# Kernel tuning notes

Hardware: AMD Instinct MI355X
Metric: run time of the kernel (lower is better)

## Reference

```python
import jax, jax.numpy as jnp
import numpy as np

N = 20000      # nodes
E = 160000     # edges
F_IN = 128     # num_node_features
D = 128        # embedding_size (out_channels)
H = 4          # heads
NEG = 0.2      # GATv2Conv negative_slope
N_LAYERS = 3


def setup_inputs() -> dict:
    key = jax.random.key(0)
    ks = jax.random.split(key, 12)
    s = 0.05
    return {
        "x": jax.random.normal(ks[0], (N, F_IN), jnp.float32),
        "edge_index": jax.random.randint(ks[1], (2, E), 0, N, jnp.int64),
        "edge_attr": jax.random.normal(ks[2], (E, 2), jnp.float32),
        "Wf": jax.random.normal(ks[3], (F_IN, D), jnp.float32) * s,
        "bf": jnp.zeros((D,), jnp.float32),
        "Wl": jax.random.normal(ks[4], (D, H * D), jnp.float32) * s,
        "bl": jnp.zeros((H * D,), jnp.float32),
        "Wr": jax.random.normal(ks[5], (D, H * D), jnp.float32) * s,
        "br": jnp.zeros((H * D,), jnp.float32),
        "We": jax.random.normal(ks[6], (2, H * D), jnp.float32) * s,
        "att": jax.random.normal(ks[7], (H, D), jnp.float32) * s,
        "bias_out": jnp.zeros((D,), jnp.float32),
    }


def reference(x, edge_index, edge_attr, Wf, bf, Wl, bl, Wr, br, We, att, bias_out):
    src, dst = edge_index[0], edge_index[1]

    # add_self_loops with fill_value='mean': self-loop edge_attr = mean of
    # incoming edge_attr per node (0 where a node has no incoming edges)
    ea_sum = jax.ops.segment_sum(edge_attr, dst, num_segments=N)            # [N,2]
    cnt = jax.ops.segment_sum(jnp.ones((E,), edge_attr.dtype), dst, num_segments=N)
    loop_attr = ea_sum / jnp.maximum(cnt, 1.0)[:, None]
    loop_idx = jnp.arange(N, dtype=src.dtype)
    fsrc = jnp.concatenate([src, loop_idx])                                  # [E+N]
    fdst = jnp.concatenate([dst, loop_idx])
    fea = jnp.concatenate([edge_attr, loop_attr], axis=0)                    # [E+N,2]

    ee = (fea @ We).reshape(-1, H, D)                                        # [E+N,H,D]

    def gatv2_layer(h):
        xl = (h @ Wl + bl).reshape(N, H, D)   # lin_l -> source-side / message
        xr = (h @ Wr + br).reshape(N, H, D)   # lin_r -> target-side
        e = jax.nn.leaky_relu(xl[fsrc] + xr[fdst] + ee, NEG)                 # [E+N,H,D]
        logits = jnp.einsum('ehd,hd->eh', e, att)                            # [E+N,H]
        m = jax.ops.segment_max(logits, fdst, num_segments=N)                # [N,H]
        w = jnp.exp(logits - m[fdst])
        denom = jax.ops.segment_sum(w, fdst, num_segments=N)                 # [N,H]
        alpha = w / denom[fdst]                                              # segment softmax
        msg = xl[fsrc] * alpha[..., None]                                    # [E+N,H,D]
        out = jax.ops.segment_sum(msg, fdst, num_segments=N)                 # [N,H,D]
        return out.mean(axis=1) + bias_out                                   # concat=False

    h = x @ Wf + bf
    for _ in range(N_LAYERS):
        h = jax.nn.leaky_relu(gatv2_layer(h), 0.01)  # F.leaky_relu default slope
    return h
```

## Files before the change

### kernel.cpp

```cpp
#include <hip/hip_runtime.h>
#include <hip/hip_bf16.h>

#define NN 20000
#define NE 160000
#define EF (NE + NN)
#define DD 128
#define HH 4
#define NPA (NN * DD)
#define NPW (1024 * 128 + 128 * 128 + 1024)
#define DEGB ((NE + 255) / 256)

typedef unsigned short u16;
typedef unsigned int u32;

using short8  = __attribute__((ext_vector_type(8))) short;
using float4v = __attribute__((ext_vector_type(4))) float;

__device__ __forceinline__ float bf2f(u16 u) {
    union { u32 i; float f; } c;
    c.i = ((u32)u) << 16;
    return c.f;
}
__device__ __forceinline__ u16 f2bf(float f) {
    union { float f; u32 u; } c;
    c.f = f;
    u32 u = c.u;
    u32 r = (u + 0x7fffu + ((u >> 16) & 1u)) >> 16;
    return (u16)r;
}


__global__ void k_zero_i(int* __restrict__ p, int n) {
    int i = blockIdx.x * blockDim.x + threadIdx.x;
    if (i < n) p[i] = 0;
}

__global__ void k_zero_f(float* __restrict__ p, int n) {
    int i = blockIdx.x * blockDim.x + threadIdx.x;
    if (i < n) p[i] = 0.f;
}


__global__ void k_degpack(const int* __restrict__ ei, const float* __restrict__ ea,
                          const float* __restrict__ x,
                          const float* __restrict__ Wl, const float* __restrict__ Wr,
                          const float* __restrict__ bl, const float* __restrict__ br,
                          const float* __restrict__ Wf,
                          int* __restrict__ cnt, float* __restrict__ ea_sum,
                          u16* __restrict__ Axh, u16* __restrict__ Axl,
                          u16* __restrict__ W2Th, u16* __restrict__ W2Tl,
                          u16* __restrict__ WfTh, u16* __restrict__ WfTl,
                          float* __restrict__ bias2) {
    int gb = blockIdx.x;
    if (gb < DEGB) {
        int e = gb * 256 + threadIdx.x;
        if (e >= NE) return;
        int t = ei[NE + e];
        atomicAdd(&cnt[t], 1);
        atomicAdd(&ea_sum[t * 2 + 0], ea[e * 2 + 0]);
        atomicAdd(&ea_sum[t * 2 + 1], ea[e * 2 + 1]);
        return;
    }
    int i = (gb - DEGB) * 256 + threadIdx.x;
    if (i < NPA) {
        float a = x[i];
        u16 h = f2bf(a);
        Axh[i] = h;
        Axl[i] = f2bf(a - bf2f(h));
        return;
    }
    i -= NPA;
    if (i < 1024 * 128) {
        int n = i >> 7, k = i & 127;
        float w = (n < 512) ? Wl[k * 512 + n] : Wr[k * 512 + (n - 512)];
        u16 h = f2bf(w);
        W2Th[n * 128 + k] = h;
        W2Tl[n * 128 + k] = f2bf(w - bf2f(h));
    } else if (i < 1024 * 128 + 128 * 128) {
        int u = i - 1024 * 128;
        int n = u >> 7, k = u & 127;
        float w = Wf[k * 128 + n];
        u16 h = f2bf(w);
        WfTh[n * 128 + k] = h;
        WfTl[n * 128 + k] = f2bf(w - bf2f(h));
    } else if (i < NPW) {
        int n = i - (1024 * 128 + 128 * 128);
        bias2[n] = (n < 512) ? bl[n] : br[n - 512];
    }
}


__global__ void k_scan(const int* __restrict__ cnt, int* __restrict__ rowptr) {
    __shared__ int wsum[16];
    __shared__ int s_base;
    int tid = threadIdx.x;
    int w = tid >> 6, l = tid & 63;
    if (tid == 0) { s_base = 0; rowptr[0] = 0; }
    __syncthreads();
    const int chunks = (NN + 1023) / 1024;
    for (int c = 0; c < chunks; ++c) {
        int i = c * 1024 + tid;
        int v = (i < NN) ? (cnt[i] + 1) : 0;
        #pragma unroll
        for (int off = 1; off < 64; off <<= 1) {
            int u = __shfl_up(v, off, 64);
            if (l >= off) v += u;
        }
        if (l == 63) wsum[w] = v;
        __syncthreads();
        if (w == 0) {
            int s = (l < 16) ? wsum[l] : 0;
            #pragma unroll
            for (int off = 1; off < 16; off <<= 1) {
                int u = __shfl_up(s, off, 64);
                if (l >= off) s += u;
            }
            if (l < 16) wsum[l] = s;
        }
        __syncthreads();
        int waveoff = (w > 0) ? wsum[w - 1] : 0;
        int incl = s_base + waveoff + v;
        if (i < NN) rowptr[i + 1] = incl;
        __syncthreads();
        if (tid == 1023) s_base = incl;
        __syncthreads();
    }
}


__global__ void k_fill(const int* __restrict__ ei, const float* __restrict__ ea,
                       const int* __restrict__ rowptr, int* __restrict__ fillc,
                       const int* __restrict__ cnt, const float* __restrict__ ea_sum,
                       int* __restrict__ srcs,
                       float* __restrict__ fa0, float* __restrict__ fa1) {
    int e = blockIdx.x * blockDim.x + threadIdx.x;
    if (e < NE) {
        int s = ei[e], t = ei[NE + e];
        int pos = atomicAdd(&fillc[t], 1);
        int slot = rowptr[t] + pos;
        srcs[slot] = s;
        fa0[slot] = ea[e * 2];
        fa1[slot] = ea[e * 2 + 1];
    } else if (e < NE + NN) {
        int n = e - NE;
        int slot = rowptr[n + 1] - 1;
        srcs[slot] = n;
        float c = fmaxf((float)cnt[n], 1.f);
        fa0[slot] = ea_sum[n * 2 + 0] / c;
        fa1[slot] = ea_sum[n * 2 + 1] / c;
    }
}


template<int SPLIT>
__global__ __launch_bounds__(256, 3) void k_mgemm(
        const u16* __restrict__ Ahg, const u16* __restrict__ Alg,
        const u16* __restrict__ BTh, const u16* __restrict__ BTl,
        const float* __restrict__ bias, float* __restrict__ C1,
        float* __restrict__ C2,
        u16* __restrict__ Oh, u16* __restrict__ Ol, int M) {
    constexpr int KS = 136;
    __shared__ u16 sAh[64 * KS], sBh[64 * KS], sBl[64 * KS];
    int m0 = blockIdx.y * 64;
    int t = threadIdx.x;
    int lane = t & 63;
    int wm = (t >> 6) & 1;
    int wn = t >> 7;
    int fm = lane & 15;
    int q8 = (lane >> 4) * 8;

    short8 fal[4][2];
    #pragma unroll
    for (int i = 0; i < 2; ++i) {
        const u16* p = Alg + (size_t)(m0 + wm * 32 + i * 16 + fm) * 128 + q8;
        #pragma unroll
        for (int kk = 0; kk < 4; ++kk)
            fal[kk][i] = *(const short8*)(p + kk * 32);
    }

    #pragma unroll
    for (int i = 0; i < 4; ++i) {
        int c = t + 256 * i;
        int row = c >> 4, ko = (c & 15) * 8;
        int gm = m0 + row;
        short8 va = {0, 0, 0, 0, 0, 0, 0, 0};
        if (gm < M) va = *(const short8*)&Ahg[gm * 128 + ko];
        *(short8*)&sAh[row * KS + ko] = va;
    }

    for (int bb = 0; bb < 2; ++bb) {
        int n0 = (blockIdx.x * 2 + bb) * 64;
        __syncthreads();
        #pragma unroll
        for (int i = 0; i < 4; ++i) {
            int c = t + 256 * i;
            int row = c >> 4, ko = (c & 15) * 8;
            int gn = n0 + row;
            *(short8*)&sBh[row * KS + ko] = *(const short8*)&BTh[gn * 128 + ko];
            *(short8*)&sBl[row * KS + ko] = *(const short8*)&BTl[gn * 128 + ko];
        }
        __syncthreads();

        float4v zz = {0.f, 0.f, 0.f, 0.f};
        float4v acc[2][2];
        acc[0][0] = zz; acc[0][1] = zz; acc[1][0] = zz; acc[1][1] = zz;

        #pragma unroll
        for (int k0 = 0; k0 < 128; k0 += 32) {
            short8 fah[2], fbh[2], fbl[2];
            #pragma unroll
            for (int i = 0; i < 2; ++i) {
                int mr = wm * 32 + i * 16 + fm;
                fah[i] = *(const short8*)&sAh[mr * KS + k0 + q8];
                int nr = wn * 32 + i * 16 + fm;
                fbh[i] = *(const short8*)&sBh[nr * KS + k0 + q8];
                fbl[i] = *(const short8*)&sBl[nr * KS + k0 + q8];
            }
            #pragma unroll
            for (int i = 0; i < 2; ++i)
                #pragma unroll
                for (int j = 0; j < 2; ++j) {
                    acc[i][j] = __builtin_amdgcn_mfma_f32_16x16x32_bf16(fah[i], fbh[j], acc[i][j], 0, 0, 0);
                    acc[i][j] = __builtin_amdgcn_mfma_f32_16x16x32_bf16(fah[i], fbl[j], acc[i][j], 0, 0, 0);
                    acc[i][j] = __builtin_amdgcn_mfma_f32_16x16x32_bf16(fal[k0 >> 5][i], fbh[j], acc[i][j], 0, 0, 0);
                }
        }

        float* Cout = (n0 < 512) ? C1 : C2;
        int cofs = (n0 < 512) ? 0 : 512;
        #pragma unroll
        for (int i = 0; i < 2; ++i) {
            #pragma unroll
            for (int j = 0; j < 2; ++j) {
                int gn = n0 + wn * 32 + j * 16 + fm;
                float bv = bias[gn];
                #pragma unroll
                for (int r = 0; r < 4; ++r) {
                    int gm = m0 + wm * 32 + i * 16 + (lane >> 4) * 4 + r;
                    if (gm < M) {
                        float v = acc[i][j][r] + bv;
                        if (SPLIT) {
                            u16 h = f2bf(v);
                            Oh[gm * 128 + gn] = h;
                            Ol[gm * 128 + gn] = f2bf(v - bf2f(h));
                        } else {
                            Cout[gm * 512 + gn - cofs] = v;
                        }
                    }
                }
            }
        }
    }
}


__global__ __launch_bounds__(256) void k_gat(
        const int* __restrict__ rowptr, const int* __restrict__ srcs,
        const float* __restrict__ fa0, const float* __restrict__ fa1,
        const float* __restrict__ xl, const float* __restrict__ xr,
        const float* __restrict__ We, const float* __restrict__ att,
        const float* __restrict__ bias_out,
        u16* __restrict__ Oh, u16* __restrict__ Ol,
        float* __restrict__ outp, int last) {
    int n = blockIdx.x * 4 + (threadIdx.x >> 6);
    if (n >= NN) return;
    int l = threadIdx.x & 63;
    int d0 = l * 8;
    float xrv[8], we0[8], we1[8], atv[8];
    {
        float4 a = *reinterpret_cast<const float4*>(&xr[(size_t)n * 512 + d0]);
        float4 b = *reinterpret_cast<const float4*>(&xr[(size_t)n * 512 + d0 + 4]);
        xrv[0]=a.x; xrv[1]=a.y; xrv[2]=a.z; xrv[3]=a.w;
        xrv[4]=b.x; xrv[5]=b.y; xrv[6]=b.z; xrv[7]=b.w;
        a = *reinterpret_cast<const float4*>(&We[d0]);
        b = *reinterpret_cast<const float4*>(&We[d0 + 4]);
        we0[0]=a.x; we0[1]=a.y; we0[2]=a.z; we0[3]=a.w;
        we0[4]=b.x; we0[5]=b.y; we0[6]=b.z; we0[7]=b.w;
        a = *reinterpret_cast<const float4*>(&We[512 + d0]);
        b = *reinterpret_cast<const float4*>(&We[512 + d0 + 4]);
        we1[0]=a.x; we1[1]=a.y; we1[2]=a.z; we1[3]=a.w;
        we1[4]=b.x; we1[5]=b.y; we1[6]=b.z; we1[7]=b.w;
        a = *reinterpret_cast<const float4*>(&att[d0]);
        b = *reinterpret_cast<const float4*>(&att[d0 + 4]);
        atv[0]=a.x; atv[1]=a.y; atv[2]=a.z; atv[3]=a.w;
        atv[4]=b.x; atv[5]=b.y; atv[6]=b.z; atv[7]=b.w;
    }
    int b0 = rowptr[n], b1 = rowptr[n + 1];
    float acc[8] = {0.f,0.f,0.f,0.f,0.f,0.f,0.f,0.f};
    float den = 0.f;
    int sNext = srcs[b0];
    for (int e = b0; e < b1; ++e) {
        int s = sNext;
        if (e + 1 < b1) sNext = srcs[e + 1];
        float f0 = fa0[e], f1 = fa1[e];
        const float* xlp = &xl[(size_t)s * 512 + d0];
        float4 a = *reinterpret_cast<const float4*>(xlp);
        float4 b = *reinterpret_cast<const float4*>(xlp + 4);
        float xv[8] = {a.x, a.y, a.z, a.w, b.x, b.y, b.z, b.w};
        float p = 0.f;
        #pragma unroll
        for (int k = 0; k < 8; ++k) {
            float v = xv[k] + xrv[k] + f0 * we0[k] + f1 * we1[k];
            v = v > 0.f ? v : 0.2f * v;
            p += v * atv[k];
        }
        p += __shfl_xor(p, 1, 64);
        p += __shfl_xor(p, 2, 64);
        p += __shfl_xor(p, 4, 64);
        p += __shfl_xor(p, 8, 64);
        float wt = __expf(p);
        den += wt;
        #pragma unroll
        for (int k = 0; k < 8; ++k) acc[k] += wt * xv[k];
    }
    float inv = 1.f / den;
    float val[8];
    #pragma unroll
    for (int k = 0; k < 8; ++k) {
        float v = acc[k] * inv;
        v += __shfl_xor(v, 16, 64);
        v += __shfl_xor(v, 32, 64);
        val[k] = v;
    }
    if (l < 16) {
        #pragma unroll
        for (int k = 0; k < 8; ++k) {
            float v = val[k] * 0.25f + bias_out[d0 + k];
            v = v > 0.f ? v : 0.01f * v;
            val[k] = v;
        }
        if (last) {
            #pragma unroll
            for (int k = 0; k < 8; ++k) outp[n * 128 + d0 + k] = val[k];
        } else {
            #pragma unroll
            for (int k = 0; k < 8; ++k) {
                u16 hv = f2bf(val[k]);
                Oh[n * 128 + d0 + k] = hv;
                Ol[n * 128 + d0 + k] = f2bf(val[k] - bf2f(hv));
            }
        }
    }
}


extern "C" void kernel_launch(void* const* d_in, const int* in_sizes, int n_in,
                              void* d_out, int out_size, void* d_ws, size_t ws_size,
                              hipStream_t stream) {
    size_t o = 0;
    auto alloc = [&](size_t bytes) { size_t cur = o; o += (bytes + 255) & ~(size_t)255; return cur; };
    size_t off_cnt    = alloc((size_t)NN * 4);
    size_t off_fillc  = alloc((size_t)NN * 4);
    size_t off_easum  = alloc((size_t)NN * 2 * 4);
    size_t off_rowptr = alloc((size_t)(NN + 1) * 4);
    size_t off_srcs   = alloc((size_t)EF * 4);
    size_t off_fa0    = alloc((size_t)EF * 4);
    size_t off_fa1    = alloc((size_t)EF * 4);
    size_t off_axh    = alloc((size_t)NN * DD * 2);
    size_t off_axl    = alloc((size_t)NN * DD * 2);
    size_t off_ah     = alloc((size_t)NN * DD * 2);
    size_t off_al     = alloc((size_t)NN * DD * 2);
    size_t off_xl     = alloc((size_t)NN * 512 * 4);
    size_t off_xr     = alloc((size_t)NN * 512 * 4);
    size_t off_w2th   = alloc((size_t)1024 * 128 * 2);
    size_t off_w2tl   = alloc((size_t)1024 * 128 * 2);
    size_t off_wfth   = alloc((size_t)128 * 128 * 2);
    size_t off_wftl   = alloc((size_t)128 * 128 * 2);
    size_t off_bias2  = alloc((size_t)1024 * 4);
    size_t need = o;

    bool ok = (n_in == 12) && d_ws != nullptr && ws_size >= need
           && out_size == NN * DD
           && in_sizes[0] == NN * DD && in_sizes[1] == 2 * NE
           && in_sizes[2] == NE * 2 && in_sizes[3] == 128 * 128
           && in_sizes[5] == 128 * 512 && in_sizes[9] == 2 * 512
           && in_sizes[10] == 4 * 128 && in_sizes[11] == 128;
    if (!ok) {
        k_zero_f<<<(NN * DD + 255) / 256, 256, 0, stream>>>((float*)d_out, NN * DD);
        return;
    }

    const float* x        = (const float*)d_in[0];
    const int*   ei       = (const int*)d_in[1];
    const float* ea       = (const float*)d_in[2];
    const float* Wf       = (const float*)d_in[3];
    const float* bf       = (const float*)d_in[4];
    const float* Wl       = (const float*)d_in[5];
    const float* bl       = (const float*)d_in[6];
    const float* Wr       = (const float*)d_in[7];
    const float* br       = (const float*)d_in[8];
    const float* We       = (const float*)d_in[9];
    const float* att      = (const float*)d_in[10];
    const float* bias_out = (const float*)d_in[11];

    char* base = (char*)d_ws;
    int*   cnt    = (int*)(base + off_cnt);
    int*   fillc  = (int*)(base + off_fillc);
    float* ea_sum = (float*)(base + off_easum);
    int*   rowptr = (int*)(base + off_rowptr);
    int*   srcs   = (int*)(base + off_srcs);
    float* fa0    = (float*)(base + off_fa0);
    float* fa1    = (float*)(base + off_fa1);
    u16*   Axh    = (u16*)(base + off_axh);
    u16*   Axl    = (u16*)(base + off_axl);
    u16*   Ah     = (u16*)(base + off_ah);
    u16*   Al     = (u16*)(base + off_al);
    float* xl     = (float*)(base + off_xl);
    float* xr     = (float*)(base + off_xr);
    u16*   W2Th   = (u16*)(base + off_w2th);
    u16*   W2Tl   = (u16*)(base + off_w2tl);
    u16*   WfTh   = (u16*)(base + off_wfth);
    u16*   WfTl   = (u16*)(base + off_wftl);
    float* bias2  = (float*)(base + off_bias2);

    int zero_ints = (int)((off_easum + (size_t)NN * 2 * 4 - off_cnt) / 4);
    k_zero_i<<<(zero_ints + 255) / 256, 256, 0, stream>>>(cnt, zero_ints);

    int packb = (NPA + NPW + 255) / 256;
    k_degpack<<<DEGB + packb, 256, 0, stream>>>(ei, ea, x, Wl, Wr, bl, br, Wf,
                                                cnt, ea_sum, Axh, Axl,
                                                W2Th, W2Tl, WfTh, WfTl, bias2);
    k_scan<<<1, 1024, 0, stream>>>(cnt, rowptr);
    k_fill<<<(NE + NN + 255) / 256, 256, 0, stream>>>(ei, ea, rowptr, fillc,
                                                      cnt, ea_sum, srcs, fa0, fa1);

    const int MT = (NN + 63) / 64;
    k_mgemm<1><<<dim3(1, MT), 256, 0, stream>>>(Axh, Axl, WfTh, WfTl,
                                                bf, nullptr, nullptr, Ah, Al, NN);

    for (int layer = 0; layer < 3; ++layer) {
        k_mgemm<0><<<dim3(8, MT), 256, 0, stream>>>(Ah, Al, W2Th, W2Tl,
                                                    bias2, xl, xr, nullptr, nullptr, NN);
        int last = (layer == 2);
        k_gat<<<(NN + 3) / 4, 256, 0, stream>>>(rowptr, srcs, fa0, fa1, xl, xr,
                                                We, att, bias_out, Ah, Al,
                                                (float*)d_out, last);
    }
}
```

Measured before the change: 463.6 us.

## Store xr as bf16 and XOR-swizzle GEMM shared-memory tiles

The GEMM now writes the target-side projection xr as bf16 instead of fp32, halving its store and load traffic, and the attention kernel converts it back to float on load. Separately, the shared-memory tiles drop the padded row stride and use an XOR swizzle of 16-byte chunks to avoid bank conflicts with less LDS. Storing xr in bf16 loses precision in the attention logits, which can shift softmax weights.

Measured after the change: 463.9 us. About the same (+0.1%).

```diff
diff --git a/kernel.cpp b/kernel.cpp
--- a/kernel.cpp
+++ b/kernel.cpp
@@ -14,6 +14,7 @@
 typedef unsigned int u32;
 
 using short8  = __attribute__((ext_vector_type(8))) short;
+using ushort8 = __attribute__((ext_vector_type(8))) unsigned short;
 using float4v = __attribute__((ext_vector_type(4))) float;
 
 __device__ __forceinline__ float bf2f(u16 u) {
@@ -157,10 +158,9 @@
         const u16* __restrict__ Ahg, const u16* __restrict__ Alg,
         const u16* __restrict__ BTh, const u16* __restrict__ BTl,
         const float* __restrict__ bias, float* __restrict__ C1,
-        float* __restrict__ C2,
+        u16* __restrict__ C2b,
         u16* __restrict__ Oh, u16* __restrict__ Ol, int M) {
-    constexpr int KS = 136;
-    __shared__ u16 sAh[64 * KS], sBh[64 * KS], sBl[64 * KS];
+    __shared__ u16 sAh[64 * 128], sBh[64 * 128], sBl[64 * 128];
     int m0 = blockIdx.y * 64;
     int t = threadIdx.x;
     int lane = t & 63;
@@ -181,12 +181,14 @@
     #pragma unroll
     for (int i = 0; i < 4; ++i) {
         int c = t + 256 * i;
-        int row = c >> 4, ko = (c & 15) * 8;
+        int row = c >> 4, ch = c & 15;
         int gm = m0 + row;
         short8 va = {0, 0, 0, 0, 0, 0, 0, 0};
-        if (gm < M) va = *(const short8*)&Ahg[gm * 128 + ko];
-        *(short8*)&sAh[row * KS + ko] = va;
-    }
+        if (gm < M) va = *(const short8*)&Ahg[gm * 128 + ch * 8];
+        *(short8*)&sAh[row * 128 + ((ch ^ (row & 15)) << 3)] = va;
+    }
+
+    int cq = q8 >> 3;
 
     for (int bb = 0; bb < 2; ++bb) {
         int n0 = (blockIdx.x * 2 + bb) * 64;
@@ -194,10 +196,11 @@
         #pragma unroll
         for (int i = 0; i < 4; ++i) {
             int c = t + 256 * i;
-            int row = c >> 4, ko = (c & 15) * 8;
+            int row = c >> 4, ch = c & 15;
             int gn = n0 + row;
-            *(short8*)&sBh[row * KS + ko] = *(const short8*)&BTh[gn * 128 + ko];
-            *(short8*)&sBl[row * KS + ko] = *(const short8*)&BTl[gn * 128 + ko];
+            int d = row * 128 + ((ch ^ (row & 15)) << 3);
+            *(short8*)&sBh[d] = *(const short8*)&BTh[gn * 128 + ch * 8];
+            *(short8*)&sBl[d] = *(const short8*)&BTl[gn * 128 + ch * 8];
         }
         __syncthreads();
 
@@ -207,14 +210,16 @@
 
         #pragma unroll
         for (int k0 = 0; k0 < 128; k0 += 32) {
+            int cl = (k0 >> 3) + cq;
+            int sw = (cl ^ fm) << 3;
             short8 fah[2], fbh[2], fbl[2];
             #pragma unroll
             for (int i = 0; i < 2; ++i) {
                 int mr = wm * 32 + i * 16 + fm;
-                fah[i] = *(const short8*)&sAh[mr * KS + k0 + q8];
+                fah[i] = *(const short8*)&sAh[mr * 128 + sw];
                 int nr = wn * 32 + i * 16 + fm;
-                fbh[i] = *(const short8*)&sBh[nr * KS + k0 + q8];
-                fbl[i] = *(const short8*)&sBl[nr * KS + k0 + q8];
+                fbh[i] = *(const short8*)&sBh[nr * 128 + sw];
+                fbl[i] = *(const short8*)&sBl[nr * 128 + sw];
             }
             #pragma unroll
             for (int i = 0; i < 2; ++i)
@@ -226,8 +231,6 @@
                 }
         }
 
-        float* Cout = (n0 < 512) ? C1 : C2;
-        int cofs = (n0 < 512) ? 0 : 512;
         #pragma unroll
         for (int i = 0; i < 2; ++i) {
             #pragma unroll
@@ -243,8 +246,10 @@
                             u16 h = f2bf(v);
                             Oh[gm * 128 + gn] = h;
                             Ol[gm * 128 + gn] = f2bf(v - bf2f(h));
+                        } else if (n0 < 512) {
+                            C1[gm * 512 + gn] = v;
                         } else {
-                            Cout[gm * 512 + gn - cofs] = v;
+                            C2b[gm * 512 + gn - 512] = f2bf(v);
                         }
                     }
                 }
@@ -257,7 +262,7 @@
 __global__ __launch_bounds__(256) void k_gat(
         const int* __restrict__ rowptr, const int* __restrict__ srcs,
         const float* __restrict__ fa0, const float* __restrict__ fa1,
-        const float* __restrict__ xl, const float* __restrict__ xr,
+        const float* __restrict__ xl, const u16* __restrict__ xr,
         const float* __restrict__ We, const float* __restrict__ att,
         const float* __restrict__ bias_out,
         u16* __restrict__ Oh, u16* __restrict__ Ol,
@@ -268,12 +273,11 @@
     int d0 = l * 8;
     float xrv[8], we0[8], we1[8], atv[8];
     {
-        float4 a = *reinterpret_cast<const float4*>(&xr[(size_t)n * 512 + d0]);
-        float4 b = *reinterpret_cast<const float4*>(&xr[(size_t)n * 512 + d0 + 4]);
-        xrv[0]=a.x; xrv[1]=a.y; xrv[2]=a.z; xrv[3]=a.w;
-        xrv[4]=b.x; xrv[5]=b.y; xrv[6]=b.z; xrv[7]=b.w;
-        a = *reinterpret_cast<const float4*>(&We[d0]);
-        b = *reinterpret_cast<const float4*>(&We[d0 + 4]);
+        ushort8 u = *reinterpret_cast<const ushort8*>(&xr[(size_t)n * 512 + d0]);
+        #pragma unroll
+        for (int k = 0; k < 8; ++k) xrv[k] = bf2f(u[k]);
+        float4 a = *reinterpret_cast<const float4*>(&We[d0]);
+        float4 b = *reinterpret_cast<const float4*>(&We[d0 + 4]);
         we0[0]=a.x; we0[1]=a.y; we0[2]=a.z; we0[3]=a.w;
         we0[4]=b.x; we0[5]=b.y; we0[6]=b.z; we0[7]=b.w;
         a = *reinterpret_cast<const float4*>(&We[512 + d0]);
@@ -361,7 +365,7 @@
     size_t off_ah     = alloc((size_t)NN * DD * 2);
     size_t off_al     = alloc((size_t)NN * DD * 2);
     size_t off_xl     = alloc((size_t)NN * 512 * 4);
-    size_t off_xr     = alloc((size_t)NN * 512 * 4);
+    size_t off_xr     = alloc((size_t)NN * 512 * 2);
     size_t off_w2th   = alloc((size_t)1024 * 128 * 2);
     size_t off_w2tl   = alloc((size_t)1024 * 128 * 2);
     size_t off_wfth   = alloc((size_t)128 * 128 * 2);
@@ -406,7 +410,7 @@
     u16*   Ah     = (u16*)(base + off_ah);
     u16*   Al     = (u16*)(base + off_al);
     float* xl     = (float*)(base + off_xl);
-    float* xr     = (float*)(base + off_xr);
+    u16*   xr     = (u16*)(base + off_xr);
     u16*   W2Th   = (u16*)(base + off_w2th);
     u16*   W2Tl   = (u16*)(base + off_w2tl);
     u16*   WfTh   = (u16*)(base + off_wfth);
```
